# Kernel tuning notes

Measured on AMD Instinct MI355X. Metric: run time of the kernel, lower is better.

## Reference

```python
import jax, jax.numpy as jnp
import numpy as np
from jax import lax

WIN = 7
K1 = 0.01
K2 = 0.03


def _box(t, w):
    # 'valid' box filter: uniform WINxWIN window, matches F.conv2d(t, w)
    return lax.conv_general_dilated(
        t, w, window_strides=(1, 1), padding='VALID',
        dimension_numbers=('NCHW', 'OIHW', 'NCHW'))


def setup_inputs() -> dict:
    key = jax.random.key(0)
    kx, ky = jax.random.split(key)
    X = jax.random.uniform(kx, (256, 1, 320, 320), dtype=jnp.float32)
    Y = jax.random.uniform(ky, (256, 1, 320, 320), dtype=jnp.float32)
    return {"X": X, "Y": Y}


def reference(X, Y):
    NP = WIN * WIN
    cov_norm = NP / (NP - 1)  # unbiased covariance correction
    w = jnp.ones((1, 1, WIN, WIN), X.dtype) / NP

    # per-sample dynamic range of the reference image Y -> [B,1,1,1]
    data_range = jnp.max(Y, axis=(1, 2, 3), keepdims=True)
    C1 = (K1 * data_range) ** 2
    C2 = (K2 * data_range) ** 2

    ux = _box(X, w)
    uy = _box(Y, w)
    uxx = _box(X * X, w)
    uyy = _box(Y * Y, w)
    uxy = _box(X * Y, w)

    vx = cov_norm * (uxx - ux * ux)
    vy = cov_norm * (uyy - uy * uy)
    vxy = cov_norm * (uxy - ux * uy)

    A1 = 2 * ux * uy + C1
    A2 = 2 * vxy + C2
    B1 = ux * ux + uy * uy + C1
    B2 = vx + vy + C2

    S = (A1 * A2) / (B1 * B2)
    S = jnp.mean(S)          # reduced=True
    return 1.0 - S           # as_loss=True
```

## Files before the change

### kernel.cpp

```cpp
#include <hip/hip_runtime.h>

#define BATCH 256
#define IMH 320
#define IMW 320
#define OUTD 314
#define NCH 9
#define RCH 36
#define ITERS 42
#define NTHR 192

__global__ __launch_bounds__(256) void k_max(const float* __restrict__ Y,
                                             unsigned* __restrict__ dr) {
    int bid = blockIdx.x;
    int b = bid >> 2, part = bid & 3;
    const float4* p = (const float4*)(Y + (size_t)b * (IMH * IMW) + part * (IMH * IMW / 4));
    float m = 0.f;
    for (int i = threadIdx.x; i < (IMH * IMW / 16); i += 256) {
        float4 v = p[i];
        m = fmaxf(m, fmaxf(fmaxf(v.x, v.y), fmaxf(v.z, v.w)));
    }
    for (int off = 32; off; off >>= 1) m = fmaxf(m, __shfl_down(m, off, 64));
    __shared__ float sm[4];
    int lane = threadIdx.x & 63, wv = threadIdx.x >> 6;
    if (lane == 0) sm[wv] = m;
    __syncthreads();
    if (threadIdx.x == 0) {
        m = fmaxf(fmaxf(sm[0], sm[1]), fmaxf(sm[2], sm[3]));
        atomicMax(dr + b, __float_as_uint(m));
    }
}

__device__ __forceinline__ float ssim_px(float hx, float hy, float hp, float hxy,
                                         float C1, float C2) {
    const float inv = 1.f / 49.f;
    const float cn  = 49.f / 48.f;
    float ux  = hx  * inv, uy = hy * inv;
    float upp = hp  * inv;
    float uxy = hxy * inv;
    float ux2 = ux * ux, uy2 = uy * uy, uxuy = ux * uy;
    float B2 = cn * (upp - ux2 - uy2) + C2;
    float A2 = 2.f * cn * (uxy - uxuy) + C2;
    float A1 = 2.f * uxuy + C1;
    float B1 = ux2 + uy2 + C1;
    return (A1 * A2) * __builtin_amdgcn_rcpf(B1 * B2);
}

__global__ __launch_bounds__(NTHR) void k_ssim(const float* __restrict__ X,
                                               const float* __restrict__ Y,
                                               const unsigned* __restrict__ dr,
                                               double* __restrict__ acc) {
    const int idx = blockIdx.x;
    const int b  = idx / NCH;
    const int rc = idx - b * NCH;
    const int t  = threadIdx.x;
    const int r0 = rc * RCH;
    const int nout = min(RCH, OUTD - r0);
    const bool act = (t < IMW / 2);
    const bool rdr = (t <= (OUTD - 2) / 2);

    const float2* Xp = (const float2*)(X + (size_t)b * (IMH * IMW));
    const float2* Yp = (const float2*)(Y + (size_t)b * (IMH * IMW));

    const float drv = __uint_as_float(dr[b]);
    const float c1s = 0.01f * drv, c2s = 0.03f * drv;
    const float C1 = c1s * c1s, C2 = c2s * c2s;

    __shared__ float2 vs[2][4][NTHR + 4];

    float2 rx[7], ry[7];
    #pragma unroll
    for (int k = 0; k < 7; ++k) { rx[k] = make_float2(0.f, 0.f); ry[k] = make_float2(0.f, 0.f); }
    float2 sx  = make_float2(0.f, 0.f), sy  = make_float2(0.f, 0.f);
    float2 sp  = make_float2(0.f, 0.f), sxy = make_float2(0.f, 0.f);
    float part = 0.f;

    #define VBODY(K, I7) {                                                     \
        const int i = (I7) + (K);                                              \
        const int r = r0 + i;                                                  \
        float2 xn = make_float2(0.f, 0.f), yn = make_float2(0.f, 0.f);         \
        if (act && r < IMH) { xn = Xp[r * (IMW/2) + t]; yn = Yp[r * (IMW/2) + t]; } \
        const float2 ox = rx[K], oy = ry[K];                                   \
        sx.x  += xn.x - ox.x;              sx.y  += xn.y - ox.y;               \
        sy.x  += yn.x - oy.x;              sy.y  += yn.y - oy.y;               \
        sp.x  += (xn.x*xn.x + yn.x*yn.x) - (ox.x*ox.x + oy.x*oy.x);            \
        sp.y  += (xn.y*xn.y + yn.y*yn.y) - (ox.y*ox.y + oy.y*oy.y);            \
        sxy.x += xn.x*yn.x - ox.x*oy.x;    sxy.y += xn.y*yn.y - ox.y*oy.y;     \
        rx[K] = xn; ry[K] = yn;                                                \
        if (i >= 6) {                                      \
            const int par = i & 1;                                             \
            if (act) { vs[par][0][t] = sx;  vs[par][1][t] = sy;                \
                       vs[par][2][t] = sp;  vs[par][3][t] = sxy; }             \
            __syncthreads();                                                   \
            if (rdr && (i - 6 < nout)) {                                       \
                float h0[4], h1[4];                                            \
                _Pragma("unroll")                                              \
                for (int q = 0; q < 4; ++q) {                                  \
                    float2 v0 = vs[par][q][t],     v1 = vs[par][q][t + 1];     \
                    float2 v2 = vs[par][q][t + 2], v3 = vs[par][q][t + 3];     \
                    float s8 = ((v0.x + v0.y) + (v1.x + v1.y))                 \
                             + ((v2.x + v2.y) + (v3.x + v3.y));                \
                    h0[q] = s8 - v3.y;             \
                    h1[q] = s8 - v0.x;             \
                }                                                              \
                part += ssim_px(h0[0], h0[1], h0[2], h0[3], C1, C2);           \
                part += ssim_px(h1[0], h1[1], h1[2], h1[3], C1, C2);           \
            }                                                                  \
        }                                                                      \
    }

    for (int i7 = 0; i7 < ITERS; i7 += 7) {
        VBODY(0, i7) VBODY(1, i7) VBODY(2, i7) VBODY(3, i7)
        VBODY(4, i7) VBODY(5, i7) VBODY(6, i7)
    }
    #undef VBODY

    for (int off = 32; off; off >>= 1) part += __shfl_down(part, off, 64);
    __shared__ float ps[3];
    const int lane = t & 63, wv = t >> 6;
    if (lane == 0) ps[wv] = part;
    __syncthreads();
    if (t == 0) atomicAdd(acc, (double)((ps[0] + ps[1]) + ps[2]));
}

__global__ void k_final(const double* __restrict__ acc, float* __restrict__ out) {
    const double cnt = (double)BATCH * (double)OUTD * (double)OUTD;
    out[0] = (float)(1.0 - acc[0] / cnt);
}

extern "C" void kernel_launch(void* const* d_in, const int* in_sizes, int n_in,
                              void* d_out, int out_size, void* d_ws, size_t ws_size,
                              hipStream_t stream) {
    const float* X = (const float*)d_in[0];
    const float* Y = (const float*)d_in[1];
    float* out = (float*)d_out;

    unsigned* dr = (unsigned*)d_ws;
    double* acc  = (double*)((char*)d_ws + 1024);

    hipMemsetAsync(d_ws, 0, 2048, stream);
    k_max <<<BATCH * 4, 256, 0, stream>>>(Y, dr);
    k_ssim<<<BATCH * NCH, NTHR, 0, stream>>>(X, Y, dr, acc);
    k_final<<<1, 1, 0, stream>>>(acc, out);
}
```

Measured before the change: 281.3 us.

## Replace shared-memory row exchange and block barriers with per-wave ds_bpermute

Each wave now owns its own overlapping column tile, with a 3-float2 halo recomputed redundantly at tile edges. The horizontal 7-tap sums are built from neighbouring lanes with ds_bpermute instead of being staged through a double-buffered LDS array. This removes the per-row __syncthreads across the three waves and the LDS stores. In exchange it adds redundant halo loads and vertical-sum work, uses more permute instructions per row, and masks invalid lanes at the end.

```diff
diff --git a/kernel.cpp b/kernel.cpp
--- a/kernel.cpp
+++ b/kernel.cpp
@@ -45,6 +45,10 @@
     return (A1 * A2) * __builtin_amdgcn_rcpf(B1 * B2);
 }
 
+__device__ __forceinline__ float bperm(int addr, float v) {
+    return __int_as_float(__builtin_amdgcn_ds_bpermute(addr, __float_as_int(v)));
+}
+
 __global__ __launch_bounds__(NTHR) void k_ssim(const float* __restrict__ X,
                                                const float* __restrict__ Y,
                                                const unsigned* __restrict__ dr,
@@ -53,19 +57,25 @@
     const int b  = idx / NCH;
     const int rc = idx - b * NCH;
     const int t  = threadIdx.x;
+    const int w  = t >> 6;
+    const int l  = t & 63;
     const int r0 = rc * RCH;
     const int nout = min(RCH, OUTD - r0);
-    const bool act = (t < IMW / 2);
-    const bool rdr = (t <= (OUTD - 2) / 2);
 
-    const float2* Xp = (const float2*)(X + (size_t)b * (IMH * IMW));
-    const float2* Yp = (const float2*)(Y + (size_t)b * (IMH * IMW));
+    const int in_base = (w == 0) ? 0 : (w == 1 ? 122 : 192);
+    const int lane_lo = (w == 2) ? 26 : 0;
+    const bool valid = (l >= lane_lo) && (l <= 60);
+
+    const float2* Xp = (const float2*)(X + (size_t)b * (IMH * IMW)) + (in_base >> 1) + l;
+    const float2* Yp = (const float2*)(Y + (size_t)b * (IMH * IMW)) + (in_base >> 1) + l;
+
+    const int a1 = ((l + 1) & 63) << 2;
+    const int a2 = ((l + 2) & 63) << 2;
+    const int a3 = ((l + 3) & 63) << 2;
 
     const float drv = __uint_as_float(dr[b]);
     const float c1s = 0.01f * drv, c2s = 0.03f * drv;
     const float C1 = c1s * c1s, C2 = c2s * c2s;
-
-    __shared__ float2 vs[2][4][NTHR + 4];
 
     float2 rx[7], ry[7];
     #pragma unroll
@@ -74,11 +84,20 @@
     float2 sp  = make_float2(0.f, 0.f), sxy = make_float2(0.f, 0.f);
     float part = 0.f;
 
+    #define HQ(q, h0, h1) {                                                    \
+        float s2_ = q.x + q.y;                                                 \
+        float b1_ = bperm(a1, s2_);                                            \
+        float b2_ = bperm(a2, s2_);                                            \
+        float b3_ = bperm(a3, s2_);                                            \
+        float y3_ = bperm(a3, q.y);                                            \
+        float S8_ = (s2_ + b1_) + (b2_ + b3_);                                 \
+        h0 = S8_ - y3_;  h1 = S8_ - q.x; }
+
     #define VBODY(K, I7) {                                                     \
         const int i = (I7) + (K);                                              \
         const int r = r0 + i;                                                  \
         float2 xn = make_float2(0.f, 0.f), yn = make_float2(0.f, 0.f);         \
-        if (act && r < IMH) { xn = Xp[r * (IMW/2) + t]; yn = Yp[r * (IMW/2) + t]; } \
+        if (r < IMH) { xn = Xp[r * (IMW/2)]; yn = Yp[r * (IMW/2)]; }           \
         const float2 ox = rx[K], oy = ry[K];                                   \
         sx.x  += xn.x - ox.x;              sx.y  += xn.y - ox.y;               \
         sy.x  += yn.x - oy.x;              sy.y  += yn.y - oy.y;               \
@@ -86,25 +105,15 @@
         sp.y  += (xn.y*xn.y + yn.y*yn.y) - (ox.y*ox.y + oy.y*oy.y);            \
         sxy.x += xn.x*yn.x - ox.x*oy.x;    sxy.y += xn.y*yn.y - ox.y*oy.y;     \
         rx[K] = xn; ry[K] = yn;                                                \
-        if (i >= 6) {                                      \
-            const int par = i & 1;                                             \
-            if (act) { vs[par][0][t] = sx;  vs[par][1][t] = sy;                \
-                       vs[par][2][t] = sp;  vs[par][3][t] = sxy; }             \
-            __syncthreads();                                                   \
-            if (rdr && (i - 6 < nout)) {                                       \
-                float h0[4], h1[4];                                            \
-                _Pragma("unroll")                                              \
-                for (int q = 0; q < 4; ++q) {                                  \
-                    float2 v0 = vs[par][q][t],     v1 = vs[par][q][t + 1];     \
-                    float2 v2 = vs[par][q][t + 2], v3 = vs[par][q][t + 3];     \
-                    float s8 = ((v0.x + v0.y) + (v1.x + v1.y))                 \
-                             + ((v2.x + v2.y) + (v3.x + v3.y));                \
-                    h0[q] = s8 - v3.y;             \
-                    h1[q] = s8 - v0.x;             \
-                }                                                              \
-                part += ssim_px(h0[0], h0[1], h0[2], h0[3], C1, C2);           \
-                part += ssim_px(h1[0], h1[1], h1[2], h1[3], C1, C2);           \
-            }                                                                  \
+        if (i >= 6 && (i - 6) < nout) {        \
+            float hx0,hx1,hy0,hy1,hp0,hp1,hq0,hq1;                             \
+            HQ(sx,  hx0, hx1)                                                  \
+            HQ(sy,  hy0, hy1)                                                  \
+            HQ(sp,  hp0, hp1)                                                  \
+            HQ(sxy, hq0, hq1)                                                  \
+            float s0 = ssim_px(hx0, hy0, hp0, hq0, C1, C2);                    \
+            float s1 = ssim_px(hx1, hy1, hp1, hq1, C1, C2);                    \
+            part += valid ? (s0 + s1) : 0.f;                                   \
         }                                                                      \
     }
 
@@ -113,11 +122,11 @@
         VBODY(4, i7) VBODY(5, i7) VBODY(6, i7)
     }
     #undef VBODY
+    #undef HQ
 
     for (int off = 32; off; off >>= 1) part += __shfl_down(part, off, 64);
     __shared__ float ps[3];
-    const int lane = t & 63, wv = t >> 6;
-    if (lane == 0) ps[wv] = part;
+    if (l == 0) ps[w] = part;
     __syncthreads();
     if (t == 0) atomicAdd(acc, (double)((ps[0] + ps[1]) + ps[2]));
 }
```

Result: no change. 276.6 us (-1.7%).
